# Performance work log

Hardware: AMD Instinct MI355X
Metric: run time of the kernel (lower is better)

Reference implementation:

```python
import jax, jax.numpy as jnp
import numpy as np

B, N, D = 4, 2048, 512
H, DH = 8, 64  # heads, dim_head; inner_dim = H*DH = 512
SCALE = DH ** -0.5


def setup_inputs() -> dict:
    key = jax.random.key(0)
    kx, kw = jax.random.split(key)
    x = jax.random.normal(kx, (B, N, D), dtype=jnp.float32)
    # torch Linear weight layout: [out_features=3*H*DH, in_features=D]
    W_qkv = jax.random.normal(kw, (3 * H * DH, D), dtype=jnp.float32) * 0.02
    return {"x": x, "W_qkv": W_qkv}


def reference(x, W_qkv):
    b, n, d = x.shape
    # qkv projection (no bias since qkv_bias=False)
    qkv = x @ W_qkv.T                                  # [b, n, 3*H*DH]
    qkv = qkv.reshape(b, n, 3, H, DH).transpose(2, 0, 3, 1, 4)  # [3, b, H, n, DH]
    q, k, v = qkv[0], qkv[1], qkv[2]
    # shifted query: q_cross[t] = q[t-1] for t>=1, q_cross[0] = q[0]
    q_cross = jnp.concatenate([q[:, :, :1, :], q[:, :, :-1, :]], axis=2)
    scores = jnp.einsum("bhqd,bhkd->bhqk", q_cross * SCALE, k)  # [b, H, n, n]
    attn = jax.nn.softmax(scores, axis=-1)
    out = jnp.einsum("bhqk,bhkd->bhqd", attn, v)       # [b, H, n, DH]
    out = out.transpose(0, 2, 1, 3).reshape(b, n, H * DH)
    # to_out is Dropout(0.0) -> identity in eval / p=0
    return out
```

## Files before the change

### kernel.cpp

```cpp
#include <hip/hip_runtime.h>
#include <hip/hip_bf16.h>
#include <stdint.h>

typedef __bf16 bf16_t;
typedef float floatx4 __attribute__((ext_vector_type(4)));
typedef __bf16 bf16x8 __attribute__((ext_vector_type(8)));
typedef __bf16 bf16x4 __attribute__((ext_vector_type(4)));

#define QSCALE 0.1803368801111204f

__device__ __forceinline__ void gl2lds16(const bf16_t* g, bf16_t* l) {
    __builtin_amdgcn_global_load_lds(
        (const __attribute__((address_space(1))) unsigned int*)g,
        (__attribute__((address_space(3))) unsigned int*)l,
        16, 0, 0);
}

__global__ __launch_bounds__(256) void convert_kernel(const float* __restrict__ x,
                                                      bf16_t* __restrict__ xb,
                                                      const float* __restrict__ w,
                                                      bf16_t* __restrict__ wb,
                                                      int nx4) {
    int i = blockIdx.x * 256 + threadIdx.x;
    const float* in; bf16_t* out; int j;
    if (i < nx4) { in = x; out = xb; j = i; }
    else         { in = w; out = wb; j = i - nx4; }
    float4 v = ((const float4*)in)[j];
    bf16x4 o;
    o.x = (bf16_t)v.x; o.y = (bf16_t)v.y; o.z = (bf16_t)v.z; o.w = (bf16_t)v.w;
    ((bf16x4*)out)[j] = o;
}

__global__ __launch_bounds__(256) void qkv_gemm(const bf16_t* __restrict__ X,
                                                const bf16_t* __restrict__ W,
                                                bf16_t* __restrict__ Q,
                                                bf16_t* __restrict__ K,
                                                bf16_t* __restrict__ Vt)
{
    __shared__ bf16_t As[128 * 64];
    __shared__ bf16_t Bs[128 * 64];

    const int tid  = threadIdx.x;
    const int wave = tid >> 6;
    const int lane = tid & 63;
    const int quad = lane >> 4;
    const int lrow = lane & 15;
    const int t7g  = lrow & 7;
    const int bm0 = blockIdx.x * 128;
    const int bn0 = blockIdx.y * 128;
    const int mw = (wave >> 1) * 64;
    const int nw = (wave & 1) * 64;
    const int wbase = tid & 192;

    floatx4 acc[4][4];
#pragma unroll
    for (int i = 0; i < 4; i++)
#pragma unroll
        for (int j = 0; j < 4; j++) acc[i][j] = (floatx4)0.0f;

#pragma unroll 1
    for (int kb = 0; kb < 8; ++kb) {
        const int k0 = kb * 64;
        __syncthreads();
#pragma unroll
        for (int r = 0; r < 4; ++r) {
            int c = r * 256 + tid;
            int row = c >> 3, kc = c & 7;
            int skc = kc ^ (row & 7);
            gl2lds16(X + (size_t)(bm0 + row) * 512 + k0 + skc * 8,
                     As + (size_t)(r * 256 + wbase) * 8);
        }
#pragma unroll
        for (int r = 0; r < 4; ++r) {
            int c = r * 256 + tid;
            int row = c >> 3, kc = c & 7;
            int skc = kc ^ (row & 7);
            gl2lds16(W + (size_t)(bn0 + row) * 512 + k0 + skc * 8,
                     Bs + (size_t)(r * 256 + wbase) * 8);
        }
        __syncthreads();
#pragma unroll
        for (int ks = 0; ks < 2; ++ks) {
            bf16x8 af[4], bfr[4];
#pragma unroll
            for (int mi = 0; mi < 4; mi++)
                af[mi] = *(const bf16x8*)(As + (mw + mi * 16 + lrow) * 64 + (((ks * 4 + quad) ^ t7g) << 3));
#pragma unroll
            for (int ni = 0; ni < 4; ni++)
                bfr[ni] = *(const bf16x8*)(Bs + (nw + ni * 16 + lrow) * 64 + (((ks * 4 + quad) ^ t7g) << 3));
#pragma unroll
            for (int mi = 0; mi < 4; mi++)
#pragma unroll
                for (int ni = 0; ni < 4; ni++)
                    acc[mi][ni] = __builtin_amdgcn_mfma_f32_16x16x32_bf16(af[mi], bfr[ni], acc[mi][ni], 0, 0, 0);
        }
    }

#pragma unroll
    for (int mi = 0; mi < 4; mi++) {
        int mbase = bm0 + mw + mi * 16 + quad * 4;
        int b = mbase >> 11, n = mbase & 2047;
#pragma unroll
        for (int ni = 0; ni < 4; ni++) {
            int o = bn0 + nw + ni * 16 + lrow;
            int s  = o >> 9;
            int h  = (o >> 6) & 7;
            int dh = o & 63;
            int bh = b * 8 + h;
            if (s == 2) {
                bf16x4 pv;
#pragma unroll
                for (int r = 0; r < 4; r++) pv[r] = (bf16_t)acc[mi][ni][r];
                *(bf16x4*)(Vt + ((size_t)bh * 64 + dh) * 2048 + n) = pv;
            } else if (s == 0) {
#pragma unroll
                for (int r = 0; r < 4; r++)
                    Q[((size_t)bh * 2048 + n + r) * 64 + dh] = (bf16_t)(acc[mi][ni][r] * QSCALE);
            } else {
#pragma unroll
                for (int r = 0; r < 4; r++)
                    K[((size_t)bh * 2048 + n + r) * 64 + dh] = (bf16_t)acc[mi][ni][r];
            }
        }
    }
}

__device__ __forceinline__ void stage_tile(const bf16_t* __restrict__ kb,
                                           const bf16_t* __restrict__ vb,
                                           int kt, bf16_t* ksbuf, bf16_t* vsbuf,
                                           int wave, int lane) {
#pragma unroll
    for (int part = 0; part < 4; ++part) {
        int ch  = part * 128 + wave * 64 + lane;
        int row = ch >> 3, cc = ch & 7;
        int scc = cc ^ (row & 7);
        bf16_t* ldst = ksbuf + (size_t)(part * 128 + wave * 64) * 8;
        gl2lds16(kb + ((size_t)(kt * 64 + row)) * 64 + scc * 8, ldst);
        bf16_t* ldst2 = vsbuf + (size_t)(part * 128 + wave * 64) * 8;
        gl2lds16(vb + (size_t)row * 2048 + kt * 64 + scc * 8, ldst2);
    }
}

__global__ __launch_bounds__(128) void flash_attn(const bf16_t* __restrict__ Q,
                                                  const bf16_t* __restrict__ K,
                                                  const bf16_t* __restrict__ Vt,
                                                  float* __restrict__ Out)
{
    __shared__ bf16_t Ks[2][64 * 64];
    __shared__ bf16_t Vs[2][64 * 64];
    __shared__ bf16_t Ps[2][32 * 64];

    const int tid  = threadIdx.x;
    const int wave = tid >> 6;
    const int lane = tid & 63;
    const int quad = lane >> 4;
    const int c    = lane & 15;
    const int t7   = c & 7;
    const int qt = blockIdx.x;
    const int bh = blockIdx.y;
    const int b = bh >> 3, h = bh & 7;

    bf16x8 qf[2][2];
#pragma unroll
    for (int mt = 0; mt < 2; ++mt) {
        int qg  = qt * 64 + wave * 32 + mt * 16 + c;
        int src = (qg == 0) ? 0 : qg - 1;
        const bf16_t* qbase = Q + ((size_t)bh * 2048 + src) * 64;
        qf[mt][0] = *(const bf16x8*)(qbase + quad * 8);
        qf[mt][1] = *(const bf16x8*)(qbase + 32 + quad * 8);
    }

    floatx4 o[2][4];
#pragma unroll
    for (int mt = 0; mt < 2; ++mt)
#pragma unroll
        for (int i = 0; i < 4; i++) o[mt][i] = (floatx4)0.0f;
    float lacc[2][4] = {{0.f, 0.f, 0.f, 0.f}, {0.f, 0.f, 0.f, 0.f}};

    const bf16_t* kb = K + ((size_t)bh * 2048) * 64;
    const bf16_t* vb = Vt + ((size_t)bh * 64) * 2048;
    bf16_t* pw = Ps[wave];

    stage_tile(kb, vb, 0, Ks[0], Vs[0], wave, lane);

#pragma unroll 1
    for (int kt = 0; kt < 32; ++kt) {
        const int buf = kt & 1;
        __syncthreads();
        if (kt < 31)
            stage_tile(kb, vb, kt + 1, Ks[buf ^ 1], Vs[buf ^ 1], wave, lane);

        const bf16_t* ks = Ks[buf];
        const bf16_t* vs = Vs[buf];

        floatx4 s[2][4];
        __builtin_amdgcn_s_setprio(1);
#pragma unroll
        for (int sub = 0; sub < 4; ++sub) {
            const bf16_t* krow = ks + (sub * 16 + c) * 64;
            bf16x8 kf0 = *(const bf16x8*)(krow + ((quad ^ t7) << 3));
            bf16x8 kf1 = *(const bf16x8*)(krow + (((4 + quad) ^ t7) << 3));
#pragma unroll
            for (int mt = 0; mt < 2; ++mt) {
                floatx4 t = (floatx4)0.0f;
                t = __builtin_amdgcn_mfma_f32_16x16x32_bf16(qf[mt][0], kf0, t, 0, 0, 0);
                t = __builtin_amdgcn_mfma_f32_16x16x32_bf16(qf[mt][1], kf1, t, 0, 0, 0);
                s[mt][sub] = t;
            }
        }
        __builtin_amdgcn_s_setprio(0);

#pragma unroll
        for (int mt = 0; mt < 2; ++mt)
#pragma unroll
            for (int sub = 0; sub < 4; ++sub)
#pragma unroll
                for (int r = 0; r < 4; r++) {
                    float p = __builtin_amdgcn_exp2f(s[mt][sub][r]);
                    lacc[mt][r] += p;
                    int row  = mt * 16 + quad * 4 + r;
                    int col8 = sub * 2 + (c >> 3);
                    pw[row * 64 + ((col8 ^ (row & 7)) << 3) + t7] = (bf16_t)p;
                }

        __builtin_amdgcn_s_setprio(1);
#pragma unroll
        for (int ki = 0; ki < 2; ++ki) {
            bf16x8 pf0 = *(const bf16x8*)(pw + c * 64 + (((ki * 4 + quad) ^ t7) << 3));
            bf16x8 pf1 = *(const bf16x8*)(pw + (16 + c) * 64 + (((ki * 4 + quad) ^ t7) << 3));
#pragma unroll
            for (int sub = 0; sub < 4; ++sub) {
                const bf16_t* vrow = vs + (sub * 16 + c) * 64;
                bf16x8 vf = *(const bf16x8*)(vrow + (((ki * 4 + quad) ^ t7) << 3));
                o[0][sub] = __builtin_amdgcn_mfma_f32_16x16x32_bf16(pf0, vf, o[0][sub], 0, 0, 0);
                o[1][sub] = __builtin_amdgcn_mfma_f32_16x16x32_bf16(pf1, vf, o[1][sub], 0, 0, 0);
            }
        }
        __builtin_amdgcn_s_setprio(0);
    }

    float* ob = Out + (size_t)b * 2048 * 512 + (size_t)h * 64;
#pragma unroll
    for (int mt = 0; mt < 2; ++mt) {
#pragma unroll
        for (int r = 0; r < 4; r++)
#pragma unroll
            for (int d = 1; d < 16; d <<= 1)
                lacc[mt][r] += __shfl_xor(lacc[mt][r], d, 64);

        int n0 = qt * 64 + wave * 32 + mt * 16 + quad * 4;
#pragma unroll
        for (int r = 0; r < 4; r++) {
            float inv = 1.0f / lacc[mt][r];
            float* orow = ob + (size_t)(n0 + r) * 512;
#pragma unroll
            for (int sub = 0; sub < 4; ++sub)
                orow[sub * 16 + c] = o[mt][sub][r] * inv;
        }
    }
}

extern "C" void kernel_launch(void* const* d_in, const int* in_sizes, int n_in,
                              void* d_out, int out_size, void* d_ws, size_t ws_size,
                              hipStream_t stream) {
    const float* x = (const float*)d_in[0];
    const float* w = (const float*)d_in[1];
    float* out = (float*)d_out;

    char* ws = (char*)d_ws;
    bf16_t* xb = (bf16_t*)(ws);
    bf16_t* wb = (bf16_t*)(ws + 8388608);
    bf16_t* q  = (bf16_t*)(ws + 9961472);
    bf16_t* k  = (bf16_t*)(ws + 18350080);
    bf16_t* vt = (bf16_t*)(ws + 26738688);

    convert_kernel<<<4864, 256, 0, stream>>>(x, xb, w, wb, 1048576);
    qkv_gemm<<<dim3(64, 12), 256, 0, stream>>>(xb, wb, q, k, vt);
    flash_attn<<<dim3(32, 32), 128, 0, stream>>>(q, k, vt, out);
}
```

Before: 158.1 us.

## Split key tiles across two waves per query half in flash attention

Doubles the flash attention block to four waves. Each pair of waves shares the same 32 query rows and splits every 64-key tile into two 32-key halves, so each wave does half the score and PV work per tile. At the end, partial outputs and row sums are combined through shared memory. This raises the number of waves per CU and halves per-wave serial MFMA work, at the cost of an extra LDS reduction, more barriers and duplicated Q fragment loads.

```diff
diff --git a/kernel.cpp b/kernel.cpp
--- a/kernel.cpp
+++ b/kernel.cpp
@@ -130,25 +130,25 @@
                                            int kt, bf16_t* ksbuf, bf16_t* vsbuf,
                                            int wave, int lane) {
 #pragma unroll
-    for (int part = 0; part < 4; ++part) {
-        int ch  = part * 128 + wave * 64 + lane;
+    for (int part = 0; part < 2; ++part) {
+        int ch  = part * 256 + wave * 64 + lane;
         int row = ch >> 3, cc = ch & 7;
         int scc = cc ^ (row & 7);
-        bf16_t* ldst = ksbuf + (size_t)(part * 128 + wave * 64) * 8;
+        bf16_t* ldst = ksbuf + (size_t)(part * 256 + wave * 64) * 8;
         gl2lds16(kb + ((size_t)(kt * 64 + row)) * 64 + scc * 8, ldst);
-        bf16_t* ldst2 = vsbuf + (size_t)(part * 128 + wave * 64) * 8;
+        bf16_t* ldst2 = vsbuf + (size_t)(part * 256 + wave * 64) * 8;
         gl2lds16(vb + (size_t)row * 2048 + kt * 64 + scc * 8, ldst2);
     }
 }
 
-__global__ __launch_bounds__(128) void flash_attn(const bf16_t* __restrict__ Q,
-                                                  const bf16_t* __restrict__ K,
-                                                  const bf16_t* __restrict__ Vt,
-                                                  float* __restrict__ Out)
+__global__ __launch_bounds__(256, 4) void flash_attn(const bf16_t* __restrict__ Q,
+                                                     const bf16_t* __restrict__ K,
+                                                     const bf16_t* __restrict__ Vt,
+                                                     float* __restrict__ Out)
 {
     __shared__ bf16_t Ks[2][64 * 64];
     __shared__ bf16_t Vs[2][64 * 64];
-    __shared__ bf16_t Ps[2][32 * 64];
+    __shared__ bf16_t Ps[4][32 * 32];
 
     const int tid  = threadIdx.x;
     const int wave = tid >> 6;
@@ -156,6 +156,8 @@
     const int quad = lane >> 4;
     const int c    = lane & 15;
     const int t7   = c & 7;
+    const int qhalf = wave >> 1;
+    const int khalf = wave & 1;
     const int qt = blockIdx.x;
     const int bh = blockIdx.y;
     const int b = bh >> 3, h = bh & 7;
@@ -163,7 +165,7 @@
     bf16x8 qf[2][2];
 #pragma unroll
     for (int mt = 0; mt < 2; ++mt) {
-        int qg  = qt * 64 + wave * 32 + mt * 16 + c;
+        int qg  = qt * 64 + qhalf * 32 + mt * 16 + c;
         int src = (qg == 0) ? 0 : qg - 1;
         const bf16_t* qbase = Q + ((size_t)bh * 2048 + src) * 64;
         qf[mt][0] = *(const bf16x8*)(qbase + quad * 8);
@@ -193,11 +195,11 @@
         const bf16_t* ks = Ks[buf];
         const bf16_t* vs = Vs[buf];
 
-        floatx4 s[2][4];
+        floatx4 s[2][2];
         __builtin_amdgcn_s_setprio(1);
 #pragma unroll
-        for (int sub = 0; sub < 4; ++sub) {
-            const bf16_t* krow = ks + (sub * 16 + c) * 64;
+        for (int nt = 0; nt < 2; ++nt) {
+            const bf16_t* krow = ks + (khalf * 32 + nt * 16 + c) * 64;
             bf16x8 kf0 = *(const bf16x8*)(krow + ((quad ^ t7) << 3));
             bf16x8 kf1 = *(const bf16x8*)(krow + (((4 + quad) ^ t7) << 3));
 #pragma unroll
@@ -205,7 +207,7 @@
                 floatx4 t = (floatx4)0.0f;
                 t = __builtin_amdgcn_mfma_f32_16x16x32_bf16(qf[mt][0], kf0, t, 0, 0, 0);
                 t = __builtin_amdgcn_mfma_f32_16x16x32_bf16(qf[mt][1], kf1, t, 0, 0, 0);
-                s[mt][sub] = t;
+                s[mt][nt] = t;
             }
         }
         __builtin_amdgcn_s_setprio(0);
@@ -213,49 +215,81 @@
 #pragma unroll
         for (int mt = 0; mt < 2; ++mt)
 #pragma unroll
-            for (int sub = 0; sub < 4; ++sub)
+            for (int nt = 0; nt < 2; ++nt)
 #pragma unroll
                 for (int r = 0; r < 4; r++) {
-                    float p = __builtin_amdgcn_exp2f(s[mt][sub][r]);
+                    float p = __builtin_amdgcn_exp2f(s[mt][nt][r]);
                     lacc[mt][r] += p;
                     int row  = mt * 16 + quad * 4 + r;
-                    int col8 = sub * 2 + (c >> 3);
-                    pw[row * 64 + ((col8 ^ (row & 7)) << 3) + t7] = (bf16_t)p;
+                    int colc = nt * 2 + (c >> 3);
+                    pw[row * 32 + ((colc ^ (row & 3)) << 3) + t7] = (bf16_t)p;
                 }
 
         __builtin_amdgcn_s_setprio(1);
-#pragma unroll
-        for (int ki = 0; ki < 2; ++ki) {
-            bf16x8 pf0 = *(const bf16x8*)(pw + c * 64 + (((ki * 4 + quad) ^ t7) << 3));
-            bf16x8 pf1 = *(const bf16x8*)(pw + (16 + c) * 64 + (((ki * 4 + quad) ^ t7) << 3));
-#pragma unroll
-            for (int sub = 0; sub < 4; ++sub) {
-                const bf16_t* vrow = vs + (sub * 16 + c) * 64;
-                bf16x8 vf = *(const bf16x8*)(vrow + (((ki * 4 + quad) ^ t7) << 3));
-                o[0][sub] = __builtin_amdgcn_mfma_f32_16x16x32_bf16(pf0, vf, o[0][sub], 0, 0, 0);
-                o[1][sub] = __builtin_amdgcn_mfma_f32_16x16x32_bf16(pf1, vf, o[1][sub], 0, 0, 0);
-            }
+        bf16x8 pf[2];
+#pragma unroll
+        for (int mt = 0; mt < 2; ++mt)
+            pf[mt] = *(const bf16x8*)(pw + (mt * 16 + c) * 32 + ((quad ^ (c & 3)) << 3));
+#pragma unroll
+        for (int sub = 0; sub < 4; ++sub) {
+            const bf16_t* vrow = vs + (sub * 16 + c) * 64;
+            bf16x8 vf = *(const bf16x8*)(vrow + (((khalf * 4 + quad) ^ t7) << 3));
+            o[0][sub] = __builtin_amdgcn_mfma_f32_16x16x32_bf16(pf[0], vf, o[0][sub], 0, 0, 0);
+            o[1][sub] = __builtin_amdgcn_mfma_f32_16x16x32_bf16(pf[1], vf, o[1][sub], 0, 0, 0);
         }
         __builtin_amdgcn_s_setprio(0);
     }
 
-    float* ob = Out + (size_t)b * 2048 * 512 + (size_t)h * 64;
-#pragma unroll
-    for (int mt = 0; mt < 2; ++mt) {
+#pragma unroll
+    for (int mt = 0; mt < 2; ++mt)
 #pragma unroll
         for (int r = 0; r < 4; r++)
 #pragma unroll
             for (int d = 1; d < 16; d <<= 1)
                 lacc[mt][r] += __shfl_xor(lacc[mt][r], d, 64);
 
-        int n0 = qt * 64 + wave * 32 + mt * 16 + quad * 4;
-#pragma unroll
-        for (int r = 0; r < 4; r++) {
-            float inv = 1.0f / lacc[mt][r];
-            float* orow = ob + (size_t)(n0 + r) * 512;
+    __syncthreads();
+    float* obuf = (float*)Ks;
+    float* lbuf = (float*)Ps;
+    if (khalf == 1) {
+#pragma unroll
+        for (int mt = 0; mt < 2; ++mt)
 #pragma unroll
             for (int sub = 0; sub < 4; ++sub)
-                orow[sub * 16 + c] = o[mt][sub][r] * inv;
+                *(floatx4*)(obuf + qhalf * 2048 + (mt * 4 + sub) * 256 + lane * 4) = o[mt][sub];
+        if (c == 0) {
+#pragma unroll
+            for (int mt = 0; mt < 2; ++mt)
+#pragma unroll
+                for (int r = 0; r < 4; r++)
+                    lbuf[qhalf * 32 + mt * 16 + quad * 4 + r] = lacc[mt][r];
+        }
+    }
+    __syncthreads();
+    if (khalf == 0) {
+#pragma unroll
+        for (int mt = 0; mt < 2; ++mt)
+#pragma unroll
+            for (int sub = 0; sub < 4; ++sub)
+                o[mt][sub] += *(const floatx4*)(obuf + qhalf * 2048 + (mt * 4 + sub) * 256 + lane * 4);
+#pragma unroll
+        for (int mt = 0; mt < 2; ++mt)
+#pragma unroll
+            for (int r = 0; r < 4; r++)
+                lacc[mt][r] += lbuf[qhalf * 32 + mt * 16 + quad * 4 + r];
+
+        float* ob = Out + (size_t)b * 2048 * 512 + (size_t)h * 64;
+#pragma unroll
+        for (int mt = 0; mt < 2; ++mt) {
+            int n0 = qt * 64 + qhalf * 32 + mt * 16 + quad * 4;
+#pragma unroll
+            for (int r = 0; r < 4; r++) {
+                float inv = 1.0f / lacc[mt][r];
+                float* orow = ob + (size_t)(n0 + r) * 512;
+#pragma unroll
+                for (int sub = 0; sub < 4; ++sub)
+                    orow[sub * 16 + c] = o[mt][sub][r] * inv;
+            }
         }
     }
 }
@@ -276,5 +310,5 @@
 
     convert_kernel<<<4864, 256, 0, stream>>>(x, xb, w, wb, 1048576);
     qkv_gemm<<<dim3(64, 12), 256, 0, stream>>>(xb, wb, q, k, vt);
-    flash_attn<<<dim3(32, 32), 128, 0, stream>>>(q, k, vt, out);
-}
+    flash_attn<<<dim3(32, 32), 256, 0, stream>>>(q, k, vt, out);
+}
```

New measurement: 152.9 us. 1.03x faster.
